# Performance work log

Hardware: AMD Instinct MI355X
Metric: run time of the kernel (lower is better)

The kernel has to match this reference:

```python
import jax, jax.numpy as jnp
import numpy as np
import math

D_MODEL = 1024
N_HEAD = 16
B, T = 4, 2048


def setup_inputs() -> dict:
    key = jax.random.key(0)
    ks = jax.random.split(key, 12)
    s = 1.0 / math.sqrt(D_MODEL)
    inp = {
        "q": jax.random.normal(ks[0], (B, T, D_MODEL), dtype=jnp.float32),
        "k": jax.random.normal(ks[1], (B, T, D_MODEL), dtype=jnp.float32),
        "v": jax.random.normal(ks[2], (B, T, D_MODEL), dtype=jnp.float32),
        "Wq": jax.random.uniform(ks[3], (D_MODEL, D_MODEL), jnp.float32, -s, s),
        "bq": jax.random.uniform(ks[4], (D_MODEL,), jnp.float32, -s, s),
        "Wk": jax.random.uniform(ks[5], (D_MODEL, D_MODEL), jnp.float32, -s, s),
        "bk": jax.random.uniform(ks[6], (D_MODEL,), jnp.float32, -s, s),
        "Wv": jax.random.uniform(ks[7], (D_MODEL, D_MODEL), jnp.float32, -s, s),
        "bv": jax.random.uniform(ks[8], (D_MODEL,), jnp.float32, -s, s),
        "Wo": jax.random.uniform(ks[9], (D_MODEL, D_MODEL), jnp.float32, -s, s),
        "bo": jax.random.uniform(ks[10], (D_MODEL,), jnp.float32, -s, s),
    }
    return inp


def reference(q, k, v, Wq, bq, Wk, bk, Wv, bv, Wo, bo):
    # NOTE: original module applies all three projections to `q` (k, v args unused)
    batch, time, dim = q.shape
    n_d = dim // N_HEAD
    # torch Linear: x @ W.T + b
    Q = (q @ Wq.T + bq).reshape(batch, time, N_HEAD, n_d).transpose(0, 2, 1, 3)
    K = (q @ Wk.T + bk).reshape(batch, time, N_HEAD, n_d).transpose(0, 2, 1, 3)
    V = (q @ Wv.T + bv).reshape(batch, time, N_HEAD, n_d).transpose(0, 2, 1, 3)
    # [B, H, T, T]
    score = jnp.einsum("bhqd,bhkd->bhqk", Q, K) / jnp.sqrt(jnp.float32(n_d))
    causal = jnp.tril(jnp.ones((time, time), dtype=bool))
    score = jnp.where(causal, score, -jnp.inf)
    # original uses Softmax(dim=-2): normalizes over the QUERY axis (faithful)
    attn = jax.nn.softmax(score, axis=-2)
    ctx = jnp.einsum("bhqk,bhkd->bhqd", attn, V)
    ctx = ctx.transpose(0, 2, 1, 3).reshape(batch, time, dim)
    return ctx @ Wo.T + bo
```

## Files before the change

### kernel.cpp

```cpp
#include <hip/hip_runtime.h>
#include <hip/hip_bf16.h>
#include <cstdint>
#include <cstddef>

typedef __bf16 bf16x8 __attribute__((ext_vector_type(8)));
typedef __bf16 bf16x4 __attribute__((ext_vector_type(4)));
typedef __bf16 bf16x2 __attribute__((ext_vector_type(2)));
typedef float  f32x4  __attribute__((ext_vector_type(4)));

static constexpr int TSEQ  = 2048;
static constexpr int DM    = 1024;
static constexpr int NH    = 16;
static constexpr int HD    = 64;
static constexpr int BATCH = 4;
static constexpr float SCL = 0.18033688011112042f;

__device__ __forceinline__ void gload16(const __bf16* g, __bf16* l) {
  __builtin_amdgcn_global_load_lds((const __attribute__((address_space(1))) void*)g,
                                   (__attribute__((address_space(3))) void*)l, 16, 0, 0);
}

#define PBAR()   asm volatile("s_barrier" ::: "memory")
#define LGKMN(n) asm volatile("s_waitcnt lgkmcnt(" #n ")" ::: "memory")

__global__ __launch_bounds__(256) void cvt_kernel(const float* __restrict__ in,
                                                  __bf16* __restrict__ out, int n4) {
  int i = blockIdx.x * 256 + threadIdx.x;
  if (i < n4) {
    float4 v = reinterpret_cast<const float4*>(in)[i];
    bf16x4 o;
    o[0] = (__bf16)v.x; o[1] = (__bf16)v.y; o[2] = (__bf16)v.z; o[3] = (__bf16)v.w;
    reinterpret_cast<bf16x4*>(out)[i] = o;
  }
}

__global__ __launch_bounds__(256) void cvt4_kernel(
    const float* __restrict__ a, const float* __restrict__ bsrc,
    const float* __restrict__ c, const float* __restrict__ d,
    __bf16* __restrict__ oa, __bf16* __restrict__ ob,
    __bf16* __restrict__ oc, __bf16* __restrict__ od, int n4) {
  const float* src = (blockIdx.y == 0) ? a : (blockIdx.y == 1) ? bsrc
                    : (blockIdx.y == 2) ? c : d;
  __bf16* dst = (blockIdx.y == 0) ? oa : (blockIdx.y == 1) ? ob
               : (blockIdx.y == 2) ? oc : od;
  int i = blockIdx.x * 256 + threadIdx.x;
  if (i < n4) {
    float4 v = reinterpret_cast<const float4*>(src)[i];
    bf16x4 o;
    o[0] = (__bf16)v.x; o[1] = (__bf16)v.y; o[2] = (__bf16)v.z; o[3] = (__bf16)v.w;
    reinterpret_cast<bf16x4*>(dst)[i] = o;
  }
}

__global__ __launch_bounds__(512, 2) void gemm_qkv_kernel(
    const __bf16* __restrict__ A, const __bf16* __restrict__ Wqkv,
    const float* __restrict__ b0, const float* __restrict__ b1,
    const float* __restrict__ b2, __bf16* __restrict__ QKVp) {
  __shared__ __align__(16) __bf16 lA[2 * 256 * 64];
  __shared__ __align__(16) __bf16 lB[2 * 192 * 64];
  const int flat = blockIdx.x;
  const int xcd = flat & 7, idx = flat >> 3;
  const int mi = xcd * 4 + (idx & 3);
  const int nig = idx >> 2;
  const int i0 = mi * 256, o0 = nig * 192;

  const int tid = threadIdx.x;
  const int l = tid & 63, lr = l & 15, lg = l >> 4;
  const int w = tid >> 6;
  const int wr = w >> 2, wc = w & 3;

  f32x4 acc[8][3];
  const f32x4 fzero = {0.f, 0.f, 0.f, 0.f};
#pragma unroll
  for (int mm = 0; mm < 8; ++mm)
#pragma unroll
    for (int ni = 0; ni < 3; ++ni) acc[mm][ni] = fzero;

  const int s_row = tid >> 3;
  const int s_cc  = tid & 7;
  const __bf16* Ab = A + (size_t)i0 * DM;
  const __bf16* Wb = Wqkv + (size_t)o0 * DM;

  auto stageA = [&](int buf, int kt, int h) {
#pragma unroll
    for (int rr = 0; rr < 2; ++rr) {
      int row = h * 128 + rr * 64 + s_row;
      gload16(Ab + (size_t)row * DM + kt * 64 + ((s_cc ^ (row & 7)) << 3),
              lA + buf * 16384 + (h * 128 + rr * 64) * 64 + tid * 8);
    }
  };
  auto stageB = [&](int buf, int kt, int n) {
    int row = n * 64 + s_row;
    gload16(Wb + (size_t)row * DM + kt * 64 + ((s_cc ^ (row & 7)) << 3),
            lB + buf * 12288 + n * 4096 + tid * 8);
  };
  auto rdA = [&](const __bf16* base, int row, int ks) {
    int chunk = (ks * 4 + lg) ^ (row & 7);
    return *(const bf16x8*)(base + row * 64 + chunk * 8);
  };

  const int NT = DM / 64;

#pragma unroll
  for (int h = 0; h < 2; ++h) stageA(0, 0, h);
#pragma unroll
  for (int n = 0; n < 3; ++n) stageB(0, 0, n);
#pragma unroll
  for (int h = 0; h < 2; ++h) stageA(1, 1, h);
#pragma unroll
  for (int n = 0; n < 3; ++n) stageB(1, 1, n);
  asm volatile("s_waitcnt vmcnt(7)" ::: "memory");
  PBAR();

  bf16x8 afl[4][2], afh[4][2], bfl[2][2], bfh[2];
#pragma unroll
  for (int mm = 0; mm < 4; ++mm)
#pragma unroll
    for (int ks = 0; ks < 2; ++ks)
      afl[mm][ks] = rdA(lA, wr * 128 + mm * 16 + lr, ks);
#pragma unroll
  for (int ni = 0; ni < 2; ++ni)
#pragma unroll
    for (int ks = 0; ks < 2; ++ks)
      bfl[ni][ks] = rdA(lB, wc * 48 + ni * 16 + lr, ks);

  for (int t = 0; t < NT; ++t) {
    const int cur = t & 1;
    const __bf16* cA = lA + cur * 16384;
    const __bf16* cB = lB + cur * 12288;
    const __bf16* nA = lA + (cur ^ 1) * 16384;
    const __bf16* nB = lB + (cur ^ 1) * 12288;
    const bool pre = (t + 2 < NT);
    const bool hasnext = (t + 1 < NT);

#pragma unroll
    for (int ks = 0; ks < 2; ++ks)
      bfh[ks] = rdA(cB, wc * 48 + 2 * 16 + lr, ks);
    PBAR(); LGKMN(2);
    __builtin_amdgcn_s_setprio(1);
#pragma unroll
    for (int mm = 0; mm < 4; ++mm)
#pragma unroll
      for (int ni = 0; ni < 2; ++ni)
#pragma unroll
        for (int ks = 0; ks < 2; ++ks)
          acc[mm][ni] = __builtin_amdgcn_mfma_f32_16x16x32_bf16(
              afl[mm][ks], bfl[ni][ks], acc[mm][ni], 0, 0, 0);
    __builtin_amdgcn_s_setprio(0);
    PBAR();

#pragma unroll
    for (int mm = 0; mm < 4; ++mm)
#pragma unroll
      for (int ks = 0; ks < 2; ++ks)
        afh[mm][ks] = rdA(cA, wr * 128 + (mm + 4) * 16 + lr, ks);
    if (pre) { stageB(cur, t + 2, 0); stageB(cur, t + 2, 1); }
    PBAR(); LGKMN(8);
    __builtin_amdgcn_s_setprio(1);
#pragma unroll
    for (int mm = 0; mm < 4; ++mm)
#pragma unroll
      for (int ks = 0; ks < 2; ++ks)
        acc[mm][2] = __builtin_amdgcn_mfma_f32_16x16x32_bf16(
            afl[mm][ks], bfh[ks], acc[mm][2], 0, 0, 0);
    __builtin_amdgcn_s_setprio(0);
    PBAR();

    if (pre) { stageB(cur, t + 2, 2); stageA(cur, t + 2, 0); }
    PBAR(); LGKMN(0);
    __builtin_amdgcn_s_setprio(1);
#pragma unroll
    for (int mm = 0; mm < 4; ++mm)
#pragma unroll
      for (int ni = 0; ni < 2; ++ni)
#pragma unroll
        for (int ks = 0; ks < 2; ++ks)
          acc[mm + 4][ni] = __builtin_amdgcn_mfma_f32_16x16x32_bf16(
              afh[mm][ks], bfl[ni][ks], acc[mm + 4][ni], 0, 0, 0);
    __builtin_amdgcn_s_setprio(0);
    PBAR();

    if (pre) stageA(cur, t + 2, 1);
    if (pre)                asm volatile("s_waitcnt vmcnt(7)" ::: "memory");
    else if (hasnext)       asm volatile("s_waitcnt vmcnt(0)" ::: "memory");
    PBAR();
    if (hasnext) {
#pragma unroll
      for (int mm = 0; mm < 4; ++mm)
#pragma unroll
        for (int ks = 0; ks < 2; ++ks)
          afl[mm][ks] = rdA(nA, wr * 128 + mm * 16 + lr, ks);
#pragma unroll
      for (int ni = 0; ni < 2; ++ni)
#pragma unroll
        for (int ks = 0; ks < 2; ++ks)
          bfl[ni][ks] = rdA(nB, wc * 48 + ni * 16 + lr, ks);
    }
    __builtin_amdgcn_s_setprio(1);
#pragma unroll
    for (int mm = 0; mm < 4; ++mm)
#pragma unroll
      for (int ks = 0; ks < 2; ++ks)
        acc[mm + 4][2] = __builtin_amdgcn_mfma_f32_16x16x32_bf16(
            afh[mm][ks], bfh[ks], acc[mm + 4][2], 0, 0, 0);
    __builtin_amdgcn_s_setprio(0);
    PBAR();
  }

#pragma unroll
  for (int ni = 0; ni < 3; ++ni) {
    int col = o0 + wc * 48 + ni * 16 + lr;
    int z = col >> 10, cin = col & 1023;
    const float* bp = (z == 0) ? b0 : (z == 1) ? b1 : b2;
    float bb = bp[cin];
    __bf16* O = QKVp + (size_t)z * 8192 * DM;
#pragma unroll
    for (int mm = 0; mm < 8; ++mm) {
      int row = i0 + wr * 128 + mm * 16 + lg * 4;
#pragma unroll
      for (int r = 0; r < 4; ++r)
        O[(size_t)(row + r) * DM + cin] = (__bf16)(acc[mm][ni][r] + bb);
    }
  }
}

template <typename OUT_T>
__device__ __forceinline__ void gemm_body2(
    const __bf16* __restrict__ A, const __bf16* __restrict__ W,
    const float* __restrict__ bias, OUT_T* __restrict__ C,
    int i0, int o0, __bf16* lA, __bf16* lB) {
  const int tid = threadIdx.x;
  const int l = tid & 63, lr = l & 15, lg = l >> 4;
  const int w = tid >> 6;
  const int wr = w >> 2, wc = w & 3;

  f32x4 acc[4][4];
  const f32x4 fzero = {0.f, 0.f, 0.f, 0.f};
#pragma unroll
  for (int mi = 0; mi < 4; ++mi)
#pragma unroll
    for (int ni = 0; ni < 4; ++ni) acc[mi][ni] = fzero;

  const int s_row = tid >> 3;
  const int s_cc  = tid & 7;
  const int NT = DM / 64;

  {
#pragma unroll
    for (int n = 0; n < 2; ++n) {
      int row = n * 64 + s_row;
      gload16(A + (size_t)(i0 + row) * DM + ((s_cc ^ (row & 7)) << 3),
              lA + n * 4096 + tid * 8);
    }
#pragma unroll
    for (int n = 0; n < 4; ++n) {
      int row = n * 64 + s_row;
      gload16(W + (size_t)(o0 + row) * DM + ((s_cc ^ (row & 7)) << 3),
              lB + n * 4096 + tid * 8);
    }
  }
  asm volatile("s_waitcnt vmcnt(0)" ::: "memory");
  __syncthreads();

  for (int t = 0; t < NT; ++t) {
    const int cur = t & 1;
    if (t + 1 < NT) {
      const int k0 = (t + 1) * 64;
      const int nxt = cur ^ 1;
#pragma unroll
      for (int n = 0; n < 2; ++n) {
        int row = n * 64 + s_row;
        gload16(A + (size_t)(i0 + row) * DM + k0 + ((s_cc ^ (row & 7)) << 3),
                lA + nxt * 8192 + n * 4096 + tid * 8);
      }
#pragma unroll
      for (int n = 0; n < 4; ++n) {
        int row = n * 64 + s_row;
        gload16(W + (size_t)(o0 + row) * DM + k0 + ((s_cc ^ (row & 7)) << 3),
                lB + nxt * 16384 + n * 4096 + tid * 8);
      }
    }

    const __bf16* cA = lA + cur * 8192;
    const __bf16* cB = lB + cur * 16384;

    bf16x8 af[4][2], bf_[2][2];
#pragma unroll
    for (int mi = 0; mi < 4; ++mi)
#pragma unroll
      for (int ks = 0; ks < 2; ++ks) {
        int row = wr * 64 + mi * 16 + lr;
        int chunk = (ks * 4 + lg) ^ (row & 7);
        af[mi][ks] = *(const bf16x8*)(cA + row * 64 + chunk * 8);
      }
#pragma unroll
    for (int ni = 0; ni < 2; ++ni)
#pragma unroll
      for (int ks = 0; ks < 2; ++ks) {
        int row = wc * 64 + ni * 16 + lr;
        int chunk = (ks * 4 + lg) ^ (row & 7);
        bf_[ni][ks] = *(const bf16x8*)(cB + row * 64 + chunk * 8);
      }
    __builtin_amdgcn_s_setprio(1);
#pragma unroll
    for (int mi = 0; mi < 4; ++mi)
#pragma unroll
      for (int ni = 0; ni < 2; ++ni)
#pragma unroll
        for (int ks = 0; ks < 2; ++ks)
          acc[mi][ni] = __builtin_amdgcn_mfma_f32_16x16x32_bf16(
              af[mi][ks], bf_[ni][ks], acc[mi][ni], 0, 0, 0);
    __builtin_amdgcn_s_setprio(0);

#pragma unroll
    for (int ni = 0; ni < 2; ++ni)
#pragma unroll
      for (int ks = 0; ks < 2; ++ks) {
        int row = wc * 64 + (ni + 2) * 16 + lr;
        int chunk = (ks * 4 + lg) ^ (row & 7);
        bf_[ni][ks] = *(const bf16x8*)(cB + row * 64 + chunk * 8);
      }
    __builtin_amdgcn_s_setprio(1);
#pragma unroll
    for (int mi = 0; mi < 4; ++mi)
#pragma unroll
      for (int ni = 0; ni < 2; ++ni)
#pragma unroll
        for (int ks = 0; ks < 2; ++ks)
          acc[mi][ni + 2] = __builtin_amdgcn_mfma_f32_16x16x32_bf16(
              af[mi][ks], bf_[ni][ks], acc[mi][ni + 2], 0, 0, 0);
    __builtin_amdgcn_s_setprio(0);

    if (t + 1 < NT) {
      asm volatile("s_waitcnt vmcnt(0)" ::: "memory");
      __syncthreads();
    }
  }

#pragma unroll
  for (int ni = 0; ni < 4; ++ni) {
    int col = o0 + wc * 64 + ni * 16 + lr;
    float bb = bias[col];
#pragma unroll
    for (int mi = 0; mi < 4; ++mi) {
      int row = i0 + wr * 64 + mi * 16 + lg * 4;
#pragma unroll
      for (int r = 0; r < 4; ++r)
        C[(size_t)(row + r) * DM + col] = (OUT_T)(acc[mi][ni][r] + bb);
    }
  }
}

__global__ __launch_bounds__(512, 2) void gemm_out_kernel(
    const __bf16* __restrict__ A, const __bf16* __restrict__ W,
    const float* __restrict__ bias, float* __restrict__ C) {
  __shared__ __align__(16) __bf16 lA[2 * 128 * 64];
  __shared__ __align__(16) __bf16 lB[2 * 256 * 64];
  const int flat = blockIdx.x;
  const int xcd = flat & 7, idx = flat >> 3;
  const int mi = xcd * 8 + (idx & 7);
  const int ni = idx >> 3;
  gemm_body2<float>(A, W, bias, C, mi * 128, ni * 256, lA, lB);
}

__global__ __launch_bounds__(256) void colstats_kernel(
    const __bf16* __restrict__ Q, const __bf16* __restrict__ K,
    const __bf16* __restrict__ V, __bf16* __restrict__ VT) {
  const int flat = blockIdx.x;
  const int wid = (flat & 7) * 128 + (flat >> 3);
  const int g = wid >> 4, bx = wid & 15;
  const int h = g & 15, b = g >> 4;
  const int tid = threadIdx.x;
  const int w = tid >> 6, l = tid & 63, lr = l & 15, lg = l >> 4;
  const size_t base = (size_t)b * TSEQ * DM + (size_t)h * HD;

  const int kt1 = 31 - bx, kt2 = bx;
  const int k01 = kt1 * 64, k02 = kt2 * 64;

  __shared__ float part[4][64];
  __shared__ float invc[64];

  bf16x8 kf1[4][2], kf2[4][2];
#pragma unroll
  for (int ct = 0; ct < 4; ++ct)
#pragma unroll
    for (int ks = 0; ks < 2; ++ks) {
      kf1[ct][ks] = *(const bf16x8*)(K + base + (size_t)(k01 + ct * 16 + lr) * DM +
                                     ks * 32 + lg * 8);
      kf2[ct][ks] = *(const bf16x8*)(K + base + (size_t)(k02 + ct * 16 + lr) * DM +
                                     ks * 32 + lg * 8);
    }

  float csum1[4] = {0.f, 0.f, 0.f, 0.f};
  float csum2[4] = {0.f, 0.f, 0.f, 0.f};
  const int nchunks = (TSEQ - k02) >> 4;
  for (int jj = w; jj < nchunks; jj += 4) {
    const int qrow = k02 + jj * 16;
    bf16x8 a0 = *(const bf16x8*)(Q + base + (size_t)(qrow + lr) * DM + lg * 8);
    bf16x8 a1 = *(const bf16x8*)(Q + base + (size_t)(qrow + lr) * DM + 32 + lg * 8);

    {
      const bool interior = (jj >= 4);
#pragma unroll
      for (int ct = 0; ct < 4; ++ct) {
        f32x4 s = {0.f, 0.f, 0.f, 0.f};
        s = __builtin_amdgcn_mfma_f32_16x16x32_bf16(a0, kf2[ct][0], s, 0, 0, 0);
        s = __builtin_amdgcn_mfma_f32_16x16x32_bf16(a1, kf2[ct][1], s, 0, 0, 0);
        if (interior) {
#pragma unroll
          for (int r = 0; r < 4; ++r) csum2[ct] += __builtin_amdgcn_exp2f(s[r] * SCL);
        } else {
#pragma unroll
          for (int r = 0; r < 4; ++r) {
            int ql = jj * 16 + lg * 4 + r;
            int kl = ct * 16 + lr;
            float e = __builtin_amdgcn_exp2f(s[r] * SCL);
            csum2[ct] += (ql >= kl) ? e : 0.f;
          }
        }
      }
    }
    if (qrow >= k01) {
      const bool interior = (qrow >= k01 + 64);
#pragma unroll
      for (int ct = 0; ct < 4; ++ct) {
        f32x4 s = {0.f, 0.f, 0.f, 0.f};
        s = __builtin_amdgcn_mfma_f32_16x16x32_bf16(a0, kf1[ct][0], s, 0, 0, 0);
        s = __builtin_amdgcn_mfma_f32_16x16x32_bf16(a1, kf1[ct][1], s, 0, 0, 0);
        if (interior) {
#pragma unroll
          for (int r = 0; r < 4; ++r) csum1[ct] += __builtin_amdgcn_exp2f(s[r] * SCL);
        } else {
#pragma unroll
          for (int r = 0; r < 4; ++r) {
            int ql = (qrow - k01) + lg * 4 + r;
            int kl = ct * 16 + lr;
            float e = __builtin_amdgcn_exp2f(s[r] * SCL);
            csum1[ct] += (ql >= kl) ? e : 0.f;
          }
        }
      }
    }
  }

#pragma unroll
  for (int ct = 0; ct < 4; ++ct) {
    csum1[ct] += __shfl_xor(csum1[ct], 16, 64);
    csum1[ct] += __shfl_xor(csum1[ct], 32, 64);
    csum2[ct] += __shfl_xor(csum2[ct], 16, 64);
    csum2[ct] += __shfl_xor(csum2[ct], 32, 64);
  }

  const int d = tid >> 2, gq = tid & 3;
  if (l < 16) {
#pragma unroll
    for (int ct = 0; ct < 4; ++ct) part[w][ct * 16 + l] = csum1[ct];
  }
  __syncthreads();
  if (tid < 64)
    invc[tid] = 1.0f / (part[0][tid] + part[1][tid] + part[2][tid] + part[3][tid]);
  __syncthreads();
  {
    size_t vtb = (((size_t)(b * NH + h)) * HD + d) * TSEQ + k01 + gq * 16;
#pragma unroll
    for (int kc = 0; kc < 16; kc += 2) {
      int kl = gq * 16 + kc;
      float v0 = (float)V[base + (size_t)(k01 + kl) * DM + d] * invc[kl];
      float v1 = (float)V[base + (size_t)(k01 + kl + 1) * DM + d] * invc[kl + 1];
      bf16x2 o; o[0] = (__bf16)v0; o[1] = (__bf16)v1;
      *(bf16x2*)(VT + vtb + kc) = o;
    }
  }
  __syncthreads();
  if (l < 16) {
#pragma unroll
    for (int ct = 0; ct < 4; ++ct) part[w][ct * 16 + l] = csum2[ct];
  }
  __syncthreads();
  if (tid < 64)
    invc[tid] = 1.0f / (part[0][tid] + part[1][tid] + part[2][tid] + part[3][tid]);
  __syncthreads();
  {
    size_t vtb = (((size_t)(b * NH + h)) * HD + d) * TSEQ + k02 + gq * 16;
#pragma unroll
    for (int kc = 0; kc < 16; kc += 2) {
      int kl = gq * 16 + kc;
      float v0 = (float)V[base + (size_t)(k02 + kl) * DM + d] * invc[kl];
      float v1 = (float)V[base + (size_t)(k02 + kl + 1) * DM + d] * invc[kl + 1];
      bf16x2 o; o[0] = (__bf16)v0; o[1] = (__bf16)v1;
      *(bf16x2*)(VT + vtb + kc) = o;
    }
  }
}

__device__ __forceinline__ int swz(int e) { return e ^ (((e >> 6) & 7) << 3); }

__global__ __launch_bounds__(256, 4) void ctx_kernel(
    const __bf16* __restrict__ Q, const __bf16* __restrict__ K,
    const __bf16* __restrict__ VT, __bf16* __restrict__ CTX) {
  __shared__ __align__(16) __bf16 lK[4096];
  __shared__ __align__(16) __bf16 lV[4096];
  __shared__ __align__(16) __bf16 lP[8][16 * 88];
  const int flat = blockIdx.x;
  const int wid = (flat & 7) * 128 + (flat >> 3);
  const int g = wid >> 4, bx = wid & 15;
  const int h = g & 15, b = g >> 4;
  const int tid = threadIdx.x;
  const int w = tid >> 6, l = tid & 63, lr = l & 15, lg = l >> 4;
  const size_t base = (size_t)b * TSEQ * DM + (size_t)h * HD;
  const size_t vtb = ((size_t)(b * NH + h)) * HD * TSEQ;
  __bf16* pw1 = &lP[w][0];
  __bf16* pw2 = &lP[w + 4][0];

  const int qt1 = 31 - bx, qt2 = bx;
  const int q01 = qt1 * 64, q02 = qt2 * 64;

  const int srow = w * 8 + (l >> 3);
  const int scol = (((l & 7) ^ (l >> 3)) << 3);

  bf16x8 qf1[2], qf2[2];
#pragma unroll
  for (int ks = 0; ks < 2; ++ks) {
    qf1[ks] = *(const bf16x8*)(Q + base + (size_t)(q01 + w * 16 + lr) * DM + ks * 32 + lg * 8);
    qf2[ks] = *(const bf16x8*)(Q + base + (size_t)(q02 + w * 16 + lr) * DM + ks * 32 + lg * 8);
  }

  f32x4 acc1[4], acc2[4];
  const f32x4 fzero = {0.f, 0.f, 0.f, 0.f};
#pragma unroll
  for (int dt = 0; dt < 4; ++dt) { acc1[dt] = fzero; acc2[dt] = fzero; }

  for (int kt = 0; kt <= qt1; ++kt) {
    const int k0 = kt * 64;
    const bool two = (kt <= qt2);
    __syncthreads();
#pragma unroll
    for (int n = 0; n < 2; ++n) {
      gload16(K + base + (size_t)(k0 + n * 32 + srow) * DM + scol,
              lK + n * 2048 + w * 512);
      gload16(VT + vtb + (size_t)(n * 32 + srow) * TSEQ + k0 + scol,
              lV + n * 2048 + w * 512);
    }
    asm volatile("s_waitcnt vmcnt(0)" ::: "memory");
    __syncthreads();

    const bool diag1 = (kt == qt1), diag2 = (kt == qt2);
#pragma unroll
    for (int ct = 0; ct < 4; ++ct) {
      bf16x8 kb[2];
#pragma unroll
      for (int ks = 0; ks < 2; ++ks) {
        int e = (ct * 16 + lr) * 64 + ks * 32 + lg * 8;
        kb[ks] = *(const bf16x8*)(lK + swz(e));
      }
      {
        f32x4 s = {0.f, 0.f, 0.f, 0.f};
        s = __builtin_amdgcn_mfma_f32_16x16x32_bf16(kb[0], qf1[0], s, 0, 0, 0);
        s = __builtin_amdgcn_mfma_f32_16x16x32_bf16(kb[1], qf1[1], s, 0, 0, 0);
        bf16x4 pk;
        if (diag1) {
#pragma unroll
          for (int r = 0; r < 4; ++r) {
            int ql = w * 16 + lr, kl = ct * 16 + lg * 4 + r;
            pk[r] = (__bf16)((ql >= kl) ? __builtin_amdgcn_exp2f(s[r] * SCL) : 0.f);
          }
        } else {
#pragma unroll
          for (int r = 0; r < 4; ++r)
            pk[r] = (__bf16)__builtin_amdgcn_exp2f(s[r] * SCL);
        }
        *(bf16x4*)(pw1 + lr * 88 + ct * 16 + lg * 4) = pk;
      }
      if (two) {
        f32x4 s = {0.f, 0.f, 0.f, 0.f};
        s = __builtin_amdgcn_mfma_f32_16x16x32_bf16(kb[0], qf2[0], s, 0, 0, 0);
        s = __builtin_amdgcn_mfma_f32_16x16x32_bf16(kb[1], qf2[1], s, 0, 0, 0);
        bf16x4 pk;
        if (diag2) {
#pragma unroll
          for (int r = 0; r < 4; ++r) {
            int ql = w * 16 + lr, kl = ct * 16 + lg * 4 + r;
            pk[r] = (__bf16)((ql >= kl) ? __builtin_amdgcn_exp2f(s[r] * SCL) : 0.f);
          }
        } else {
#pragma unroll
          for (int r = 0; r < 4; ++r)
            pk[r] = (__bf16)__builtin_amdgcn_exp2f(s[r] * SCL);
        }
        *(bf16x4*)(pw2 + lr * 88 + ct * 16 + lg * 4) = pk;
      }
    }
    asm volatile("" ::: "memory");

    bf16x8 pa1[2], pa2[2];
#pragma unroll
    for (int ks = 0; ks < 2; ++ks)
      pa1[ks] = *(const bf16x8*)(pw1 + lr * 88 + ks * 32 + lg * 8);
    if (two) {
#pragma unroll
      for (int ks = 0; ks < 2; ++ks)
        pa2[ks] = *(const bf16x8*)(pw2 + lr * 88 + ks * 32 + lg * 8);
    }
#pragma unroll
    for (int dt = 0; dt < 4; ++dt) {
#pragma unroll
      for (int ks = 0; ks < 2; ++ks) {
        int e = (dt * 16 + lr) * 64 + ks * 32 + lg * 8;
        bf16x8 vb8 = *(const bf16x8*)(lV + swz(e));
        acc1[dt] = __builtin_amdgcn_mfma_f32_16x16x32_bf16(pa1[ks], vb8, acc1[dt], 0, 0, 0);
        if (two)
          acc2[dt] = __builtin_amdgcn_mfma_f32_16x16x32_bf16(pa2[ks], vb8, acc2[dt], 0, 0, 0);
      }
    }
  }

#pragma unroll
  for (int dt = 0; dt < 4; ++dt)
#pragma unroll
    for (int r = 0; r < 4; ++r) {
      CTX[base + (size_t)(q01 + w * 16 + lg * 4 + r) * DM + dt * 16 + lr] = (__bf16)acc1[dt][r];
      CTX[base + (size_t)(q02 + w * 16 + lg * 4 + r) * DM + dt * 16 + lr] = (__bf16)acc2[dt][r];
    }
}

extern "C" void kernel_launch(void* const* d_in, const int* in_sizes, int n_in,
                              void* d_out, int out_size, void* d_ws, size_t ws_size,
                              hipStream_t stream) {
  const float* q  = (const float*)d_in[0];
  const float* Wq = (const float*)d_in[3];
  const float* bq = (const float*)d_in[4];
  const float* Wk = (const float*)d_in[5];
  const float* bk = (const float*)d_in[6];
  const float* Wv = (const float*)d_in[7];
  const float* bv = (const float*)d_in[8];
  const float* Wo = (const float*)d_in[9];
  const float* bo = (const float*)d_in[10];
  float* out = (float*)d_out;

  const size_t NTOK = (size_t)BATCH * TSEQ;
  char* ws = (char*)d_ws;
  __bf16* qb   = (__bf16*)ws; ws += NTOK * DM * 2;
  __bf16* Wqkv = (__bf16*)ws; ws += 3 * (size_t)DM * DM * 2;
  __bf16* Wob  = (__bf16*)ws; ws += (size_t)DM * DM * 2;
  __bf16* QKVp = (__bf16*)ws; ws += 3 * NTOK * DM * 2;
  __bf16* VT   = (__bf16*)ws; ws += (size_t)BATCH * NH * HD * TSEQ * 2;
  __bf16* CTX = qb;

  __bf16* Qp = QKVp;
  __bf16* Kp = QKVp + NTOK * DM;
  __bf16* Vp = QKVp + 2 * NTOK * DM;

  const int nq4 = (int)(NTOK * DM / 4);
  const int nw4 = DM * DM / 4;
  cvt_kernel<<<(nq4 + 255) / 256, 256, 0, stream>>>(q, qb, nq4);
  cvt4_kernel<<<dim3((nw4 + 255) / 256, 4), 256, 0, stream>>>(
      Wq, Wk, Wv, Wo, Wqkv, Wqkv + (size_t)DM * DM, Wqkv + 2 * (size_t)DM * DM, Wob, nw4);

  gemm_qkv_kernel<<<512, 512, 0, stream>>>(qb, Wqkv, bq, bk, bv, QKVp);

  colstats_kernel<<<1024, 256, 0, stream>>>(Qp, Kp, Vp, VT);
  ctx_kernel<<<1024, 256, 0, stream>>>(Qp, Kp, VT, CTX);

  gemm_out_kernel<<<256, 512, 0, stream>>>(CTX, Wob, bo, out);
}
```

Measured before the change: 209.0 us.

## Simplify QKV GEMM to 4-wave blocks with plain double-buffered prefetch

Rewrites the QKV projection GEMM to use 256 threads (4 waves) per block, each wave computing a 128x96 output tile with 8x6 accumulators. The hand-interleaved 8-wave ping-pong schedule with split MFMA phases and partial waitcnts is replaced by a simple loop: prefetch the next K tile, load all fragments, run all MFMAs, then wait and sync. This removes barrier overhead and schedule complexity but doubles per-thread registers and accumulators, halves the waves per block, and exposes LDS read latency before the MFMAs.

```diff
diff --git a/kernel.cpp b/kernel.cpp
--- a/kernel.cpp
+++ b/kernel.cpp
@@ -21,7 +21,6 @@
 }
 
 #define PBAR()   asm volatile("s_barrier" ::: "memory")
-#define LGKMN(n) asm volatile("s_waitcnt lgkmcnt(" #n ")" ::: "memory")
 
 __global__ __launch_bounds__(256) void cvt_kernel(const float* __restrict__ in,
                                                   __bf16* __restrict__ out, int n4) {
@@ -52,7 +51,7 @@
   }
 }
 
-__global__ __launch_bounds__(512, 2) void gemm_qkv_kernel(
+__global__ __launch_bounds__(256, 1) void gemm_qkv_kernel(
     const __bf16* __restrict__ A, const __bf16* __restrict__ Wqkv,
     const float* __restrict__ b0, const float* __restrict__ b1,
     const float* __restrict__ b2, __bf16* __restrict__ QKVp) {
@@ -67,34 +66,31 @@
   const int tid = threadIdx.x;
   const int l = tid & 63, lr = l & 15, lg = l >> 4;
   const int w = tid >> 6;
-  const int wr = w >> 2, wc = w & 3;
-
-  f32x4 acc[8][3];
+  const int wr = w >> 1, wc = w & 1;
+
+  f32x4 acc[8][6];
   const f32x4 fzero = {0.f, 0.f, 0.f, 0.f};
 #pragma unroll
   for (int mm = 0; mm < 8; ++mm)
 #pragma unroll
-    for (int ni = 0; ni < 3; ++ni) acc[mm][ni] = fzero;
+    for (int ni = 0; ni < 6; ++ni) acc[mm][ni] = fzero;
 
   const int s_row = tid >> 3;
   const int s_cc  = tid & 7;
   const __bf16* Ab = A + (size_t)i0 * DM;
   const __bf16* Wb = Wqkv + (size_t)o0 * DM;
 
-  auto stageA = [&](int buf, int kt, int h) {
-#pragma unroll
-    for (int rr = 0; rr < 2; ++rr) {
-      int row = h * 128 + rr * 64 + s_row;
-      gload16(Ab + (size_t)row * DM + kt * 64 + ((s_cc ^ (row & 7)) << 3),
-              lA + buf * 16384 + (h * 128 + rr * 64) * 64 + tid * 8);
-    }
+  auto stageA = [&](int buf, int kt, int rr) {
+    int row = rr * 32 + s_row;
+    gload16(Ab + (size_t)row * DM + kt * 64 + ((s_cc ^ (row & 7)) << 3),
+            lA + buf * 16384 + rr * 2048 + tid * 8);
   };
-  auto stageB = [&](int buf, int kt, int n) {
-    int row = n * 64 + s_row;
+  auto stageB = [&](int buf, int kt, int rr) {
+    int row = rr * 32 + s_row;
     gload16(Wb + (size_t)row * DM + kt * 64 + ((s_cc ^ (row & 7)) << 3),
-            lB + buf * 12288 + n * 4096 + tid * 8);
+            lB + buf * 12288 + rr * 2048 + tid * 8);
   };
-  auto rdA = [&](const __bf16* base, int row, int ks) {
+  auto rd = [&](const __bf16* base, int row, int ks) {
     int chunk = (ks * 4 + lg) ^ (row & 7);
     return *(const bf16x8*)(base + row * 64 + chunk * 8);
   };
@@ -102,114 +98,57 @@
   const int NT = DM / 64;
 
 #pragma unroll
-  for (int h = 0; h < 2; ++h) stageA(0, 0, h);
-#pragma unroll
-  for (int n = 0; n < 3; ++n) stageB(0, 0, n);
-#pragma unroll
-  for (int h = 0; h < 2; ++h) stageA(1, 1, h);
-#pragma unroll
-  for (int n = 0; n < 3; ++n) stageB(1, 1, n);
-  asm volatile("s_waitcnt vmcnt(7)" ::: "memory");
-  PBAR();
-
-  bf16x8 afl[4][2], afh[4][2], bfl[2][2], bfh[2];
-#pragma unroll
-  for (int mm = 0; mm < 4; ++mm)
-#pragma unroll
-    for (int ks = 0; ks < 2; ++ks)
-      afl[mm][ks] = rdA(lA, wr * 128 + mm * 16 + lr, ks);
-#pragma unroll
-  for (int ni = 0; ni < 2; ++ni)
-#pragma unroll
-    for (int ks = 0; ks < 2; ++ks)
-      bfl[ni][ks] = rdA(lB, wc * 48 + ni * 16 + lr, ks);
+  for (int rr = 0; rr < 8; ++rr) stageA(0, 0, rr);
+#pragma unroll
+  for (int rr = 0; rr < 6; ++rr) stageB(0, 0, rr);
+  asm volatile("s_waitcnt vmcnt(0)" ::: "memory");
+  __syncthreads();
 
   for (int t = 0; t < NT; ++t) {
     const int cur = t & 1;
+    if (t + 1 < NT) {
+      const int nxt = cur ^ 1;
+#pragma unroll
+      for (int rr = 0; rr < 8; ++rr) stageA(nxt, t + 1, rr);
+#pragma unroll
+      for (int rr = 0; rr < 6; ++rr) stageB(nxt, t + 1, rr);
+    }
+
     const __bf16* cA = lA + cur * 16384;
     const __bf16* cB = lB + cur * 12288;
-    const __bf16* nA = lA + (cur ^ 1) * 16384;
-    const __bf16* nB = lB + (cur ^ 1) * 12288;
-    const bool pre = (t + 2 < NT);
-    const bool hasnext = (t + 1 < NT);
-
-#pragma unroll
-    for (int ks = 0; ks < 2; ++ks)
-      bfh[ks] = rdA(cB, wc * 48 + 2 * 16 + lr, ks);
-    PBAR(); LGKMN(2);
+
+    bf16x8 af[8][2], bf[6][2];
+#pragma unroll
+    for (int mm = 0; mm < 8; ++mm)
+#pragma unroll
+      for (int ks = 0; ks < 2; ++ks)
+        af[mm][ks] = rd(cA, wr * 128 + mm * 16 + lr, ks);
+#pragma unroll
+    for (int ni = 0; ni < 6; ++ni)
+#pragma unroll
+      for (int ks = 0; ks < 2; ++ks)
+        bf[ni][ks] = rd(cB, wc * 96 + ni * 16 + lr, ks);
+
     __builtin_amdgcn_s_setprio(1);
 #pragma unroll
-    for (int mm = 0; mm < 4; ++mm)
-#pragma unroll
-      for (int ni = 0; ni < 2; ++ni)
+    for (int mm = 0; mm < 8; ++mm)
+#pragma unroll
+      for (int ni = 0; ni < 6; ++ni)
 #pragma unroll
         for (int ks = 0; ks < 2; ++ks)
           acc[mm][ni] = __builtin_amdgcn_mfma_f32_16x16x32_bf16(
-              afl[mm][ks], bfl[ni][ks], acc[mm][ni], 0, 0, 0);
+              af[mm][ks], bf[ni][ks], acc[mm][ni], 0, 0, 0);
     __builtin_amdgcn_s_setprio(0);
-    PBAR();
-
-#pragma unroll
-    for (int mm = 0; mm < 4; ++mm)
-#pragma unroll
-      for (int ks = 0; ks < 2; ++ks)
-        afh[mm][ks] = rdA(cA, wr * 128 + (mm + 4) * 16 + lr, ks);
-    if (pre) { stageB(cur, t + 2, 0); stageB(cur, t + 2, 1); }
-    PBAR(); LGKMN(8);
-    __builtin_amdgcn_s_setprio(1);
-#pragma unroll
-    for (int mm = 0; mm < 4; ++mm)
-#pragma unroll
-      for (int ks = 0; ks < 2; ++ks)
-        acc[mm][2] = __builtin_amdgcn_mfma_f32_16x16x32_bf16(
-            afl[mm][ks], bfh[ks], acc[mm][2], 0, 0, 0);
-    __builtin_amdgcn_s_setprio(0);
-    PBAR();
-
-    if (pre) { stageB(cur, t + 2, 2); stageA(cur, t + 2, 0); }
-    PBAR(); LGKMN(0);
-    __builtin_amdgcn_s_setprio(1);
-#pragma unroll
-    for (int mm = 0; mm < 4; ++mm)
-#pragma unroll
-      for (int ni = 0; ni < 2; ++ni)
-#pragma unroll
-        for (int ks = 0; ks < 2; ++ks)
-          acc[mm + 4][ni] = __builtin_amdgcn_mfma_f32_16x16x32_bf16(
-              afh[mm][ks], bfl[ni][ks], acc[mm + 4][ni], 0, 0, 0);
-    __builtin_amdgcn_s_setprio(0);
-    PBAR();
-
-    if (pre) stageA(cur, t + 2, 1);
-    if (pre)                asm volatile("s_waitcnt vmcnt(7)" ::: "memory");
-    else if (hasnext)       asm volatile("s_waitcnt vmcnt(0)" ::: "memory");
-    PBAR();
-    if (hasnext) {
-#pragma unroll
-      for (int mm = 0; mm < 4; ++mm)
-#pragma unroll
-        for (int ks = 0; ks < 2; ++ks)
-          afl[mm][ks] = rdA(nA, wr * 128 + mm * 16 + lr, ks);
-#pragma unroll
-      for (int ni = 0; ni < 2; ++ni)
-#pragma unroll
-        for (int ks = 0; ks < 2; ++ks)
-          bfl[ni][ks] = rdA(nB, wc * 48 + ni * 16 + lr, ks);
-    }
-    __builtin_amdgcn_s_setprio(1);
-#pragma unroll
-    for (int mm = 0; mm < 4; ++mm)
-#pragma unroll
-      for (int ks = 0; ks < 2; ++ks)
-        acc[mm + 4][2] = __builtin_amdgcn_mfma_f32_16x16x32_bf16(
-            afh[mm][ks], bfh[ks], acc[mm + 4][2], 0, 0, 0);
-    __builtin_amdgcn_s_setprio(0);
-    PBAR();
-  }
-
-#pragma unroll
-  for (int ni = 0; ni < 3; ++ni) {
-    int col = o0 + wc * 48 + ni * 16 + lr;
+
+    if (t + 1 < NT) {
+      asm volatile("s_waitcnt vmcnt(0)" ::: "memory");
+      __syncthreads();
+    }
+  }
+
+#pragma unroll
+  for (int ni = 0; ni < 6; ++ni) {
+    int col = o0 + wc * 96 + ni * 16 + lr;
     int z = col >> 10, cin = col & 1023;
     const float* bp = (z == 0) ? b0 : (z == 1) ? b1 : b2;
     float bb = bp[cin];
@@ -656,7 +595,7 @@
   cvt4_kernel<<<dim3((nw4 + 255) / 256, 4), 256, 0, stream>>>(
       Wq, Wk, Wv, Wo, Wqkv, Wqkv + (size_t)DM * DM, Wqkv + 2 * (size_t)DM * DM, Wob, nw4);
 
-  gemm_qkv_kernel<<<512, 512, 0, stream>>>(qb, Wqkv, bq, bk, bv, QKVp);
+  gemm_qkv_kernel<<<512, 256, 0, stream>>>(qb, Wqkv, bq, bk, bv, QKVp);
 
   colstats_kernel<<<1024, 256, 0, stream>>>(Qp, Kp, Vp, VT);
   ctx_kernel<<<1024, 256, 0, stream>>>(Qp, Kp, VT, CTX);
```

Result: slower. 213.5 us (+2.2%).

## Rework QKV GEMM pipeline and port four-phase pingpong schedule to output GEMM

Applied to the files above, without the earlier changes.

In the QKV projection GEMM, all fragment loads now happen within the current iteration and each MFMA phase waits on a full lgkmcnt(0), instead of prefetching the next tile's fragments across iterations. The output projection GEMM is rewritten to use the same four-quadrant schedule: a 2-deep global_load_lds prefetch pipeline, global loads staged between MFMA phases, and barriers with s_setprio around each phase. The wave-to-quadrant mapping is also changed so each wave covers split row and column halves. The goal is to overlap global loads with compute in the output GEMM and simplify register pressure in the QKV GEMM. In exchange, the QKV GEMM loses its LDS-read overlap, and the extra barriers may add stalls.

```diff
diff --git a/kernel.cpp b/kernel.cpp
--- a/kernel.cpp
+++ b/kernel.cpp
@@ -20,8 +20,8 @@
                                    (__attribute__((address_space(3))) void*)l, 16, 0, 0);
 }
 
-#define PBAR()   asm volatile("s_barrier" ::: "memory")
-#define LGKMN(n) asm volatile("s_waitcnt lgkmcnt(" #n ")" ::: "memory")
+#define PBAR()  asm volatile("s_barrier" ::: "memory")
+#define LGKM()  asm volatile("s_waitcnt lgkmcnt(0)" ::: "memory")
 
 __global__ __launch_bounds__(256) void cvt_kernel(const float* __restrict__ in,
                                                   __bf16* __restrict__ out, int n4) {
@@ -112,31 +112,25 @@
   asm volatile("s_waitcnt vmcnt(7)" ::: "memory");
   PBAR();
 
-  bf16x8 afl[4][2], afh[4][2], bfl[2][2], bfh[2];
-#pragma unroll
-  for (int mm = 0; mm < 4; ++mm)
-#pragma unroll
-    for (int ks = 0; ks < 2; ++ks)
-      afl[mm][ks] = rdA(lA, wr * 128 + mm * 16 + lr, ks);
-#pragma unroll
-  for (int ni = 0; ni < 2; ++ni)
-#pragma unroll
-    for (int ks = 0; ks < 2; ++ks)
-      bfl[ni][ks] = rdA(lB, wc * 48 + ni * 16 + lr, ks);
-
   for (int t = 0; t < NT; ++t) {
     const int cur = t & 1;
     const __bf16* cA = lA + cur * 16384;
     const __bf16* cB = lB + cur * 12288;
-    const __bf16* nA = lA + (cur ^ 1) * 16384;
-    const __bf16* nB = lB + (cur ^ 1) * 12288;
     const bool pre = (t + 2 < NT);
-    const bool hasnext = (t + 1 < NT);
-
-#pragma unroll
-    for (int ks = 0; ks < 2; ++ks)
-      bfh[ks] = rdA(cB, wc * 48 + 2 * 16 + lr, ks);
-    PBAR(); LGKMN(2);
+
+    bf16x8 afl[4][2], afh[4][2], bfl[2][2], bfh[2];
+
+#pragma unroll
+    for (int mm = 0; mm < 4; ++mm)
+#pragma unroll
+      for (int ks = 0; ks < 2; ++ks)
+        afl[mm][ks] = rdA(cA, wr * 128 + mm * 16 + lr, ks);
+#pragma unroll
+    for (int ni = 0; ni < 2; ++ni)
+#pragma unroll
+      for (int ks = 0; ks < 2; ++ks)
+        bfl[ni][ks] = rdA(cB, wc * 48 + ni * 16 + lr, ks);
+    PBAR(); LGKM();
     __builtin_amdgcn_s_setprio(1);
 #pragma unroll
     for (int mm = 0; mm < 4; ++mm)
@@ -150,12 +144,10 @@
     PBAR();
 
 #pragma unroll
-    for (int mm = 0; mm < 4; ++mm)
-#pragma unroll
-      for (int ks = 0; ks < 2; ++ks)
-        afh[mm][ks] = rdA(cA, wr * 128 + (mm + 4) * 16 + lr, ks);
+    for (int ks = 0; ks < 2; ++ks)
+      bfh[ks] = rdA(cB, wc * 48 + 2 * 16 + lr, ks);
     if (pre) { stageB(cur, t + 2, 0); stageB(cur, t + 2, 1); }
-    PBAR(); LGKMN(8);
+    PBAR(); LGKM();
     __builtin_amdgcn_s_setprio(1);
 #pragma unroll
     for (int mm = 0; mm < 4; ++mm)
@@ -166,8 +158,13 @@
     __builtin_amdgcn_s_setprio(0);
     PBAR();
 
+#pragma unroll
+    for (int mm = 0; mm < 4; ++mm)
+#pragma unroll
+      for (int ks = 0; ks < 2; ++ks)
+        afh[mm][ks] = rdA(cA, wr * 128 + (mm + 4) * 16 + lr, ks);
     if (pre) { stageB(cur, t + 2, 2); stageA(cur, t + 2, 0); }
-    PBAR(); LGKMN(0);
+    PBAR(); LGKM();
     __builtin_amdgcn_s_setprio(1);
 #pragma unroll
     for (int mm = 0; mm < 4; ++mm)
@@ -182,20 +179,8 @@
 
     if (pre) stageA(cur, t + 2, 1);
     if (pre)                asm volatile("s_waitcnt vmcnt(7)" ::: "memory");
-    else if (hasnext)       asm volatile("s_waitcnt vmcnt(0)" ::: "memory");
-    PBAR();
-    if (hasnext) {
-#pragma unroll
-      for (int mm = 0; mm < 4; ++mm)
-#pragma unroll
-        for (int ks = 0; ks < 2; ++ks)
-          afl[mm][ks] = rdA(nA, wr * 128 + mm * 16 + lr, ks);
-#pragma unroll
-      for (int ni = 0; ni < 2; ++ni)
-#pragma unroll
-        for (int ks = 0; ks < 2; ++ks)
-          bfl[ni][ks] = rdA(nB, wc * 48 + ni * 16 + lr, ks);
-    }
+    else if (t + 1 < NT)    asm volatile("s_waitcnt vmcnt(0)" ::: "memory");
+    PBAR();
     __builtin_amdgcn_s_setprio(1);
 #pragma unroll
     for (int mm = 0; mm < 4; ++mm)
@@ -220,133 +205,6 @@
 #pragma unroll
       for (int r = 0; r < 4; ++r)
         O[(size_t)(row + r) * DM + cin] = (__bf16)(acc[mm][ni][r] + bb);
-    }
-  }
-}
-
-template <typename OUT_T>
-__device__ __forceinline__ void gemm_body2(
-    const __bf16* __restrict__ A, const __bf16* __restrict__ W,
-    const float* __restrict__ bias, OUT_T* __restrict__ C,
-    int i0, int o0, __bf16* lA, __bf16* lB) {
-  const int tid = threadIdx.x;
-  const int l = tid & 63, lr = l & 15, lg = l >> 4;
-  const int w = tid >> 6;
-  const int wr = w >> 2, wc = w & 3;
-
-  f32x4 acc[4][4];
-  const f32x4 fzero = {0.f, 0.f, 0.f, 0.f};
-#pragma unroll
-  for (int mi = 0; mi < 4; ++mi)
-#pragma unroll
-    for (int ni = 0; ni < 4; ++ni) acc[mi][ni] = fzero;
-
-  const int s_row = tid >> 3;
-  const int s_cc  = tid & 7;
-  const int NT = DM / 64;
-
-  {
-#pragma unroll
-    for (int n = 0; n < 2; ++n) {
-      int row = n * 64 + s_row;
-      gload16(A + (size_t)(i0 + row) * DM + ((s_cc ^ (row & 7)) << 3),
-              lA + n * 4096 + tid * 8);
-    }
-#pragma unroll
-    for (int n = 0; n < 4; ++n) {
-      int row = n * 64 + s_row;
-      gload16(W + (size_t)(o0 + row) * DM + ((s_cc ^ (row & 7)) << 3),
-              lB + n * 4096 + tid * 8);
-    }
-  }
-  asm volatile("s_waitcnt vmcnt(0)" ::: "memory");
-  __syncthreads();
-
-  for (int t = 0; t < NT; ++t) {
-    const int cur = t & 1;
-    if (t + 1 < NT) {
-      const int k0 = (t + 1) * 64;
-      const int nxt = cur ^ 1;
-#pragma unroll
-      for (int n = 0; n < 2; ++n) {
-        int row = n * 64 + s_row;
-        gload16(A + (size_t)(i0 + row) * DM + k0 + ((s_cc ^ (row & 7)) << 3),
-                lA + nxt * 8192 + n * 4096 + tid * 8);
-      }
-#pragma unroll
-      for (int n = 0; n < 4; ++n) {
-        int row = n * 64 + s_row;
-        gload16(W + (size_t)(o0 + row) * DM + k0 + ((s_cc ^ (row & 7)) << 3),
-                lB + nxt * 16384 + n * 4096 + tid * 8);
-      }
-    }
-
-    const __bf16* cA = lA + cur * 8192;
-    const __bf16* cB = lB + cur * 16384;
-
-    bf16x8 af[4][2], bf_[2][2];
-#pragma unroll
-    for (int mi = 0; mi < 4; ++mi)
-#pragma unroll
-      for (int ks = 0; ks < 2; ++ks) {
-        int row = wr * 64 + mi * 16 + lr;
-        int chunk = (ks * 4 + lg) ^ (row & 7);
-        af[mi][ks] = *(const bf16x8*)(cA + row * 64 + chunk * 8);
-      }
-#pragma unroll
-    for (int ni = 0; ni < 2; ++ni)
-#pragma unroll
-      for (int ks = 0; ks < 2; ++ks) {
-        int row = wc * 64 + ni * 16 + lr;
-        int chunk = (ks * 4 + lg) ^ (row & 7);
-        bf_[ni][ks] = *(const bf16x8*)(cB + row * 64 + chunk * 8);
-      }
-    __builtin_amdgcn_s_setprio(1);
-#pragma unroll
-    for (int mi = 0; mi < 4; ++mi)
-#pragma unroll
-      for (int ni = 0; ni < 2; ++ni)
-#pragma unroll
-        for (int ks = 0; ks < 2; ++ks)
-          acc[mi][ni] = __builtin_amdgcn_mfma_f32_16x16x32_bf16(
-              af[mi][ks], bf_[ni][ks], acc[mi][ni], 0, 0, 0);
-    __builtin_amdgcn_s_setprio(0);
-
-#pragma unroll
-    for (int ni = 0; ni < 2; ++ni)
-#pragma unroll
-      for (int ks = 0; ks < 2; ++ks) {
-        int row = wc * 64 + (ni + 2) * 16 + lr;
-        int chunk = (ks * 4 + lg) ^ (row & 7);
-        bf_[ni][ks] = *(const bf16x8*)(cB + row * 64 + chunk * 8);
-      }
-    __builtin_amdgcn_s_setprio(1);
-#pragma unroll
-    for (int mi = 0; mi < 4; ++mi)
-#pragma unroll
-      for (int ni = 0; ni < 2; ++ni)
-#pragma unroll
-        for (int ks = 0; ks < 2; ++ks)
-          acc[mi][ni + 2] = __builtin_amdgcn_mfma_f32_16x16x32_bf16(
-              af[mi][ks], bf_[ni][ks], acc[mi][ni + 2], 0, 0, 0);
-    __builtin_amdgcn_s_setprio(0);
-
-    if (t + 1 < NT) {
-      asm volatile("s_waitcnt vmcnt(0)" ::: "memory");
-      __syncthreads();
-    }
-  }
-
-#pragma unroll
-  for (int ni = 0; ni < 4; ++ni) {
-    int col = o0 + wc * 64 + ni * 16 + lr;
-    float bb = bias[col];
-#pragma unroll
-    for (int mi = 0; mi < 4; ++mi) {
-      int row = i0 + wr * 64 + mi * 16 + lg * 4;
-#pragma unroll
-      for (int r = 0; r < 4; ++r)
-        C[(size_t)(row + r) * DM + col] = (OUT_T)(acc[mi][ni][r] + bb);
     }
   }
 }
@@ -359,8 +217,153 @@
   const int flat = blockIdx.x;
   const int xcd = flat & 7, idx = flat >> 3;
   const int mi = xcd * 8 + (idx & 7);
-  const int ni = idx >> 3;
-  gemm_body2<float>(A, W, bias, C, mi * 128, ni * 256, lA, lB);
+  const int nig = idx >> 3;
+  const int i0 = mi * 128, o0 = nig * 256;
+
+  const int tid = threadIdx.x;
+  const int l = tid & 63, lr = l & 15, lg = l >> 4;
+  const int w = tid >> 6;
+  const int wr = w >> 2, wc = w & 3;
+
+  f32x4 acc[4][4];
+  const f32x4 fzero = {0.f, 0.f, 0.f, 0.f};
+#pragma unroll
+  for (int mm = 0; mm < 4; ++mm)
+#pragma unroll
+    for (int ni = 0; ni < 4; ++ni) acc[mm][ni] = fzero;
+
+  const int s_row = tid >> 3;
+  const int s_cc  = tid & 7;
+  const __bf16* Ab = A + (size_t)i0 * DM;
+  const __bf16* Wb = W + (size_t)o0 * DM;
+
+  auto stageA = [&](int buf, int kt, int h) {
+    int row = h * 64 + s_row;
+    gload16(Ab + (size_t)row * DM + kt * 64 + ((s_cc ^ (row & 7)) << 3),
+            lA + buf * 8192 + h * 4096 + tid * 8);
+  };
+  auto stageB = [&](int buf, int kt, int h) {
+#pragma unroll
+    for (int rr = 0; rr < 2; ++rr) {
+      int row = h * 128 + rr * 64 + s_row;
+      gload16(Wb + (size_t)row * DM + kt * 64 + ((s_cc ^ (row & 7)) << 3),
+              lB + buf * 16384 + (h * 128 + rr * 64) * 64 + tid * 8);
+    }
+  };
+  auto rd = [&](const __bf16* base, int row, int ks) {
+    int chunk = (ks * 4 + lg) ^ (row & 7);
+    return *(const bf16x8*)(base + row * 64 + chunk * 8);
+  };
+
+  const int NT = DM / 64;
+
+#pragma unroll
+  for (int h = 0; h < 2; ++h) { stageA(0, 0, h); stageB(0, 0, h); }
+#pragma unroll
+  for (int h = 0; h < 2; ++h) { stageA(1, 1, h); stageB(1, 1, h); }
+  asm volatile("s_waitcnt vmcnt(6)" ::: "memory");
+  PBAR();
+
+  for (int t = 0; t < NT; ++t) {
+    const int cur = t & 1;
+    const __bf16* cA = lA + cur * 8192;
+    const __bf16* cB = lB + cur * 16384;
+    const bool pre = (t + 2 < NT);
+
+    bf16x8 afl[2][2], afh[2][2], bfl[2][2], bfh[2][2];
+
+#pragma unroll
+    for (int mm = 0; mm < 2; ++mm)
+#pragma unroll
+      for (int ks = 0; ks < 2; ++ks)
+        afl[mm][ks] = rd(cA, wr * 32 + mm * 16 + lr, ks);
+#pragma unroll
+    for (int ni = 0; ni < 2; ++ni)
+#pragma unroll
+      for (int ks = 0; ks < 2; ++ks)
+        bfl[ni][ks] = rd(cB, wc * 32 + ni * 16 + lr, ks);
+    PBAR(); LGKM();
+    __builtin_amdgcn_s_setprio(1);
+#pragma unroll
+    for (int mm = 0; mm < 2; ++mm)
+#pragma unroll
+      for (int ni = 0; ni < 2; ++ni)
+#pragma unroll
+        for (int ks = 0; ks < 2; ++ks)
+          acc[mm][ni] = __builtin_amdgcn_mfma_f32_16x16x32_bf16(
+              afl[mm][ks], bfl[ni][ks], acc[mm][ni], 0, 0, 0);
+    __builtin_amdgcn_s_setprio(0);
+    PBAR();
+
+#pragma unroll
+    for (int ni = 0; ni < 2; ++ni)
+#pragma unroll
+      for (int ks = 0; ks < 2; ++ks)
+        bfh[ni][ks] = rd(cB, 128 + wc * 32 + ni * 16 + lr, ks);
+    if (pre) stageB(cur, t + 2, 0);
+    PBAR(); LGKM();
+    __builtin_amdgcn_s_setprio(1);
+#pragma unroll
+    for (int mm = 0; mm < 2; ++mm)
+#pragma unroll
+      for (int ni = 0; ni < 2; ++ni)
+#pragma unroll
+        for (int ks = 0; ks < 2; ++ks)
+          acc[mm][ni + 2] = __builtin_amdgcn_mfma_f32_16x16x32_bf16(
+              afl[mm][ks], bfh[ni][ks], acc[mm][ni + 2], 0, 0, 0);
+    __builtin_amdgcn_s_setprio(0);
+    PBAR();
+
+#pragma unroll
+    for (int mm = 0; mm < 2; ++mm)
+#pragma unroll
+      for (int ks = 0; ks < 2; ++ks)
+        afh[mm][ks] = rd(cA, 64 + wr * 32 + mm * 16 + lr, ks);
+    if (pre) { stageA(cur, t + 2, 0); stageB(cur, t + 2, 1); }
+    PBAR(); LGKM();
+    __builtin_amdgcn_s_setprio(1);
+#pragma unroll
+    for (int mm = 0; mm < 2; ++mm)
+#pragma unroll
+      for (int ni = 0; ni < 2; ++ni)
+#pragma unroll
+        for (int ks = 0; ks < 2; ++ks)
+          acc[mm + 2][ni] = __builtin_amdgcn_mfma_f32_16x16x32_bf16(
+              afh[mm][ks], bfl[ni][ks], acc[mm + 2][ni], 0, 0, 0);
+    __builtin_amdgcn_s_setprio(0);
+    PBAR();
+
+    if (pre) stageA(cur, t + 2, 1);
+    if (pre)                asm volatile("s_waitcnt vmcnt(6)" ::: "memory");
+    else if (t + 1 < NT)    asm volatile("s_waitcnt vmcnt(0)" ::: "memory");
+    PBAR();
+    __builtin_amdgcn_s_setprio(1);
+#pragma unroll
+    for (int mm = 0; mm < 2; ++mm)
+#pragma unroll
+      for (int ni = 0; ni < 2; ++ni)
+#pragma unroll
+        for (int ks = 0; ks < 2; ++ks)
+          acc[mm + 2][ni + 2] = __builtin_amdgcn_mfma_f32_16x16x32_bf16(
+              afh[mm][ks], bfh[ni][ks], acc[mm + 2][ni + 2], 0, 0, 0);
+    __builtin_amdgcn_s_setprio(0);
+    PBAR();
+  }
+
+#pragma unroll
+  for (int ni = 0; ni < 4; ++ni) {
+    int colb = (ni < 2) ? (wc * 32 + ni * 16) : (128 + wc * 32 + (ni - 2) * 16);
+    int col = o0 + colb + lr;
+    float bb = bias[col];
+#pragma unroll
+    for (int mm = 0; mm < 4; ++mm) {
+      int rowb = (mm < 2) ? (wr * 32 + mm * 16) : (64 + wr * 32 + (mm - 2) * 16);
+      int row = i0 + rowb + lg * 4;
+#pragma unroll
+      for (int r = 0; r < 4; ++r)
+        C[(size_t)(row + r) * DM + col] = acc[mm][ni][r] + bb;
+    }
+  }
 }
 
 __global__ __launch_bounds__(256) void colstats_kernel(
```

Measured after the change: 204.5 us. 2.1% less time.
